# Optimization experiments

Hardware: AMD Instinct MI355X
Metric: run time of the kernel (lower is better)

## Reference

```python
import jax, jax.numpy as jnp
import numpy as np

# Model dims (match init_kwargs)
B, S = 2, 2048          # batch, seq_len
H = 1024                # hidden_size
D = 2048                # expert_hidden_dim
E = 8                   # num_experts
K = 2                   # num_experts_per_tok (top_k)


def setup_inputs() -> dict:
    key = jax.random.key(0)
    k_x, k_g, k_w1, k_w2 = jax.random.split(key, 4)
    x = jax.random.normal(k_x, (B, S, H), jnp.float32)
    # router gate: Linear(H, E, bias=False)
    gate_w = jax.random.normal(k_g, (H, E), jnp.float32) / jnp.sqrt(H).astype(jnp.float32)
    # per-expert FFN params stacked on leading expert axis
    W1 = jax.random.normal(k_w1, (E, H, D), jnp.float32) / jnp.sqrt(H).astype(jnp.float32)
    b1 = jnp.zeros((E, D), jnp.float32)
    W2 = jax.random.normal(k_w2, (E, D, H), jnp.float32) / jnp.sqrt(D).astype(jnp.float32)
    b2 = jnp.zeros((E, H), jnp.float32)
    return {"x": x, "gate_w": gate_w, "W1": W1, "b1": b1, "W2": W2, "b2": b2}


def reference(x, gate_w, W1, b1, W2, b2):
    # --- router ---
    logits = jnp.einsum('bsh,he->bse', x, gate_w)            # [B,S,E]
    probs = jax.nn.softmax(logits, axis=-1)                  # [B,S,E]
    topk_p, idx = jax.lax.top_k(probs, K)                    # [B,S,K] each
    topk_p = topk_p / topk_p.sum(axis=-1, keepdims=True)     # renormalize over top-k
    one_hot = jax.nn.one_hot(idx, E, dtype=probs.dtype)      # [B,S,K,E]
    # combine weight per (token, expert); topk indices are distinct so this
    # equals the original's masked-sum of router_probs_flat * expert_mask
    combine = jnp.einsum('bske,bsk->bse', one_hot, topk_p)   # [B,S,E]

    # --- aux load-balancing loss (faithful to original reductions) ---
    tokens_per_expert = one_hot.sum(axis=-2).mean(axis=0)    # [S,E]
    avg_prob_per_expert = probs.mean(axis=(0, 1))            # [E]
    aux_loss = E * (tokens_per_expert * avg_prob_per_expert).sum()

    # --- experts: dense-equivalent of gather-FFN-scatter (tokens with
    # combine weight 0 contribute 0, matching the masked loop) ---
    out = jnp.zeros_like(x)
    for e in range(E):  # fixed small loop over structurally distinct experts
        h = jax.nn.gelu(jnp.einsum('bsh,hd->bsd', x, W1[e]) + b1[e], approximate=False)
        out = out + combine[..., e:e + 1] * (jnp.einsum('bsd,dh->bsh', h, W2[e]) + b2[e])
    return out, aux_loss
```

## Files before the change

kernel.cpp:

```cpp
#include <hip/hip_runtime.h>
#include <hip/hip_bf16.h>

#define NTOK 4096
#define HD   1024
#define DD   2048
#define NE   8
#define SLOTS (2*NTOK)

typedef unsigned short u16;
typedef unsigned int   u32;
typedef __attribute__((ext_vector_type(8))) __bf16 bf16x8;
typedef __attribute__((ext_vector_type(4))) float  f32x4;

__device__ __forceinline__ float bf2f(u16 u) {
    u32 v = ((u32)u) << 16;
    return __uint_as_float(v);
}
__device__ __forceinline__ u16 f2bf(float f) {
    __hip_bfloat16 h = __float2bfloat16(f);
    return *reinterpret_cast<u16*>(&h);
}

__device__ __forceinline__ void gload_lds16(const void* g, void* l) {
    __builtin_amdgcn_global_load_lds(
        (__attribute__((address_space(1))) void*)g,
        (__attribute__((address_space(3))) void*)l,
        16, 0, 0);
}

__device__ __forceinline__ float gelu_f(float v) {
    float x = 0.7978845608028654f * (v + 0.044715f * v * v * v);
    float e = exp2f(x * 2.8853900817779268f);
    float th = 1.f - 2.f * __builtin_amdgcn_rcpf(e + 1.f);
    return 0.5f * v * (1.f + th);
}

__global__ __launch_bounds__(256) void cvt2_k(
        const float* __restrict__ W1, const float* __restrict__ W2,
        u16* __restrict__ W1t, u16* __restrict__ W2t) {
    int z = blockIdx.z;
    const float* src; u16* dst; int R, C;
    if (z < NE) { src = W1 + (size_t)z * HD * DD;        dst = W1t + (size_t)z * HD * DD;        R = HD; C = DD; }
    else        { src = W2 + (size_t)(z - NE) * DD * HD; dst = W2t + (size_t)(z - NE) * DD * HD; R = DD; C = HD; }
    int tcols = C >> 6;
    int r0 = (blockIdx.x / tcols) * 64;
    int c0 = (blockIdx.x % tcols) * 64;

    __shared__ u16 tile[64][68];
    int tid = threadIdx.x;
    int rr  = tid >> 4;
    int cc4 = (tid & 15) * 4;
#pragma unroll
    for (int j = 0; j < 4; ++j) {
        int r = rr + j * 16;
        float4 v = *reinterpret_cast<const float4*>(src + (size_t)(r0 + r) * C + c0 + cc4);
        tile[r][cc4 + 0] = f2bf(v.x); tile[r][cc4 + 1] = f2bf(v.y);
        tile[r][cc4 + 2] = f2bf(v.z); tile[r][cc4 + 3] = f2bf(v.w);
    }
    __syncthreads();
    int cc = tid >> 3, sl = tid & 7;
#pragma unroll
    for (int p = 0; p < 2; ++p) {
        int c = p * 32 + cc;
        u16 tmp[8];
#pragma unroll
        for (int k = 0; k < 8; ++k) tmp[k] = tile[sl * 8 + k][c];
        *reinterpret_cast<uint4*>(dst + (size_t)(c0 + c) * R + r0 + sl * 8) =
            *reinterpret_cast<uint4*>(tmp);
    }
}

__global__ __launch_bounds__(256) void router_k(
        const float* __restrict__ x, const float* __restrict__ gw,
        u16* __restrict__ xb,
        int* __restrict__ counts, float* __restrict__ sum_probs,
        int* __restrict__ tk_idx, float* __restrict__ tk_w) {
    __shared__ int   bcnt[NE];
    __shared__ float bprob[NE];
    int tid = threadIdx.x;
    if (tid < NE) { bcnt[tid] = 0; bprob[tid] = 0.f; }
    __syncthreads();

    int gtid = blockIdx.x * 256 + tid;
    int t    = gtid >> 6;
    int lane = gtid & 63;

    float acc[NE] = {0.f,0.f,0.f,0.f,0.f,0.f,0.f,0.f};
    const float* xr = x + (size_t)t * HD;
    u16* xbr = xb + (size_t)t * HD;
#pragma unroll
    for (int i = 0; i < HD / 64; ++i) {
        int h = lane + i * 64;
        float xv = xr[h];
        xbr[h] = f2bf(xv);
        const float4* g = reinterpret_cast<const float4*>(gw + (size_t)h * NE);
        float4 g0 = g[0], g1 = g[1];
        acc[0] = fmaf(xv, g0.x, acc[0]); acc[1] = fmaf(xv, g0.y, acc[1]);
        acc[2] = fmaf(xv, g0.z, acc[2]); acc[3] = fmaf(xv, g0.w, acc[3]);
        acc[4] = fmaf(xv, g1.x, acc[4]); acc[5] = fmaf(xv, g1.y, acc[5]);
        acc[6] = fmaf(xv, g1.z, acc[6]); acc[7] = fmaf(xv, g1.w, acc[7]);
    }
#pragma unroll
    for (int off = 32; off >= 1; off >>= 1) {
#pragma unroll
        for (int e = 0; e < NE; ++e) acc[e] += __shfl_xor(acc[e], off);
    }
    float m = acc[0];
#pragma unroll
    for (int e = 1; e < NE; ++e) m = fmaxf(m, acc[e]);
    float p[NE]; float s = 0.f;
#pragma unroll
    for (int e = 0; e < NE; ++e) { p[e] = expf(acc[e] - m); s += p[e]; }
    float inv = 1.f / s;

    int i1 = 0; float v1 = p[0];
#pragma unroll
    for (int e = 1; e < NE; ++e) if (p[e] > v1) { v1 = p[e]; i1 = e; }
    int i2 = -1; float v2 = -1.f;
#pragma unroll
    for (int e = 0; e < NE; ++e) if (e != i1 && p[e] > v2) { v2 = p[e]; i2 = e; }
    float wsum = v1 + v2;

    if (lane < NE) atomicAdd(&bprob[lane], p[lane] * inv);
    if (lane == 0) {
        atomicAdd(&bcnt[i1], 1);
        atomicAdd(&bcnt[i2], 1);
        tk_idx[2 * t]     = i1;  tk_idx[2 * t + 1] = i2;
        tk_w[2 * t]       = v1 / wsum;
        tk_w[2 * t + 1]   = v2 / wsum;
    }
    __syncthreads();
    if (tid < NE) {
        if (bcnt[tid]) atomicAdd(&counts[tid], bcnt[tid]);
        atomicAdd(&sum_probs[tid], bprob[tid]);
    }
}

__global__ __launch_bounds__(256) void scatter_k(
        const int* __restrict__ tk_idx, const int* __restrict__ counts,
        int* __restrict__ cursor, int* __restrict__ slot_tok,
        int* __restrict__ inv_slot, int* __restrict__ offsets) {
    __shared__ int off[NE];
    if (threadIdx.x == 0) {
        int o = 0;
        for (int e = 0; e < NE; ++e) { off[e] = o; o += counts[e]; }
        if (blockIdx.x == 0)
            for (int e = 0; e < NE; ++e) offsets[e] = off[e];
    }
    __syncthreads();
    int t = blockIdx.x * 256 + threadIdx.x;
    if (t >= NTOK) return;
#pragma unroll
    for (int k = 0; k < 2; ++k) {
        int e = tk_idx[2 * t + k];
        int pos = atomicAdd(&cursor[e], 1);
        int s = off[e] + pos;
        slot_tok[s] = t;
        inv_slot[2 * t + k] = s;
    }
}

template<int KD, bool GATHER, bool GELU>
__global__ __launch_bounds__(256) void gemm_dense_k(
        const u16* __restrict__ A,
        const u16* __restrict__ Bt,
        const float* __restrict__ bias,
        const int* __restrict__ counts, const int* __restrict__ offsets,
        const int* __restrict__ slot_tok,
        u16* __restrict__ outb, int ND) {
    int mb = blockIdx.y;
    int e = -1, m0 = 0, accb = 0;
#pragma unroll
    for (int ee = 0; ee < NE; ++ee) {
        int nb = (counts[ee] + 127) >> 7;
        if (e < 0 && mb < accb + nb) { e = ee; m0 = (mb - accb) * 128; }
        accb += nb;
    }
    if (e < 0) return;
    int cnt = counts[e], base = offsets[e];
    int n0 = blockIdx.x * 128;

    __shared__ u16 As[128 * 64];
    __shared__ u16 Bs[128 * 64];
    __shared__ int ids[128];

    int tid  = threadIdx.x;
    int lane = tid & 63;
    int w    = tid >> 6;
    int wr   = w >> 1, wc = w & 1;
    int lrow = lane & 15, khi = lane >> 4;

    if constexpr (GATHER) {
        if (tid < 128) ids[tid] = (m0 + tid < cnt) ? slot_tok[base + m0 + tid] : 0;
    }
    __syncthreads();

    const u16* Bte = Bt + (size_t)e * (size_t)ND * KD;
    int srow = tid >> 3;
    int sslot = tid & 7;

    const u16 *gA[4], *gB[4];
#pragma unroll
    for (int j = 0; j < 4; ++j) {
        int r = j * 32 + srow;
        size_t gr;
        if constexpr (GATHER) gr = (size_t)ids[r];
        else                  gr = (size_t)(base + m0 + r);
        gA[j] = A   + gr * KD                + ((sslot ^ (r & 7)) << 3);
        gB[j] = Bte + (size_t)(n0 + r) * KD  + ((sslot ^ (r & 7)) << 3);
    }

    f32x4 acc[4][4];
#pragma unroll
    for (int m = 0; m < 4; ++m)
#pragma unroll
        for (int n = 0; n < 4; ++n) acc[m][n] = {0.f, 0.f, 0.f, 0.f};

    constexpr int NK = KD / 64;
#pragma unroll 1
    for (int t = 0; t < NK; ++t) {
#pragma unroll
        for (int j = 0; j < 4; ++j) {
            gload_lds16(gA[j] + t * 64, (char*)As + j * 4096 + tid * 16);
            gload_lds16(gB[j] + t * 64, (char*)Bs + j * 4096 + tid * 16);
        }
        __syncthreads();
#pragma unroll
        for (int ks = 0; ks < 2; ++ks) {
            int slot = ks * 4 + khi;
            bf16x8 af[4], bv[4];
#pragma unroll
            for (int m = 0; m < 4; ++m) {
                int r = wr * 64 + m * 16 + lrow;
                af[m] = *reinterpret_cast<const bf16x8*>(
                    &As[r * 64 + ((slot ^ (r & 7)) << 3)]);
            }
#pragma unroll
            for (int n = 0; n < 4; ++n) {
                int r = wc * 64 + n * 16 + lrow;
                bv[n] = *reinterpret_cast<const bf16x8*>(
                    &Bs[r * 64 + ((slot ^ (r & 7)) << 3)]);
            }
            __builtin_amdgcn_s_setprio(1);
#pragma unroll
            for (int m = 0; m < 4; ++m)
#pragma unroll
                for (int n = 0; n < 4; ++n)
                    acc[m][n] = __builtin_amdgcn_mfma_f32_16x16x32_bf16(
                        af[m], bv[n], acc[m][n], 0, 0, 0);
            __builtin_amdgcn_s_setprio(0);
        }
        __syncthreads();
    }

    constexpr int PST = 72;
    u16* patch = As + w * 16 * PST;
    float bvals[4];
    if constexpr (GELU) {
#pragma unroll
        for (int n = 0; n < 4; ++n)
            bvals[n] = bias[(size_t)e * ND + n0 + wc * 64 + n * 16 + lrow];
    }
#pragma unroll
    for (int m = 0; m < 4; ++m) {
#pragma unroll
        for (int n = 0; n < 4; ++n)
#pragma unroll
            for (int i = 0; i < 4; ++i) {
                float v = acc[m][n][i];
                if constexpr (GELU) {
                    v += bvals[n];
                    v = gelu_f(v);
                }
                patch[(khi * 4 + i) * PST + n * 16 + lrow] = f2bf(v);
            }
        __syncthreads();
        int prow = lane >> 3, sl = lane & 7;
#pragma unroll
        for (int p = 0; p < 2; ++p) {
            int row  = p * 8 + prow;
            uint4 q = *reinterpret_cast<const uint4*>(&patch[row * PST + sl * 8]);
            int grow = m0 + wr * 64 + m * 16 + row;
            if (grow < cnt)
                *reinterpret_cast<uint4*>(
                    outb + (size_t)(base + grow) * ND + n0 + wc * 64 + sl * 8) = q;
        }
        __syncthreads();
    }
}

template<int KD>
__global__ __launch_bounds__(256) void gemm_n64_k(
        const u16* __restrict__ A,
        const u16* __restrict__ Bt,
        const int* __restrict__ counts, const int* __restrict__ offsets,
        u16* __restrict__ outb, int ND) {
    int mb = blockIdx.y;
    int e = -1, m0 = 0, accb = 0;
#pragma unroll
    for (int ee = 0; ee < NE; ++ee) {
        int nb = (counts[ee] + 127) >> 7;
        if (e < 0 && mb < accb + nb) { e = ee; m0 = (mb - accb) * 128; }
        accb += nb;
    }
    if (e < 0) return;
    int cnt = counts[e], base = offsets[e];
    int n0 = blockIdx.x * 64;

    __shared__ u16 As[128 * 64];
    __shared__ u16 Bs[64 * 64];

    int tid  = threadIdx.x;
    int lane = tid & 63;
    int w    = tid >> 6;
    int wr   = w >> 1, wc = w & 1;
    int lrow = lane & 15, khi = lane >> 4;

    const u16* Bte = Bt + (size_t)e * (size_t)ND * KD;
    int srow = tid >> 3;
    int sslot = tid & 7;

    const u16 *gA[4], *gB[2];
#pragma unroll
    for (int j = 0; j < 4; ++j) {
        int r = j * 32 + srow;
        gA[j] = A + (size_t)(base + m0 + r) * KD + ((sslot ^ (r & 7)) << 3);
    }
#pragma unroll
    for (int j = 0; j < 2; ++j) {
        int r = j * 32 + srow;
        gB[j] = Bte + (size_t)(n0 + r) * KD + ((sslot ^ (r & 7)) << 3);
    }

    f32x4 acc[4][2];
#pragma unroll
    for (int m = 0; m < 4; ++m)
#pragma unroll
        for (int n = 0; n < 2; ++n) acc[m][n] = {0.f, 0.f, 0.f, 0.f};

    constexpr int NK = KD / 64;
#pragma unroll 1
    for (int t = 0; t < NK; ++t) {
#pragma unroll
        for (int j = 0; j < 4; ++j)
            gload_lds16(gA[j] + t * 64, (char*)As + j * 4096 + tid * 16);
#pragma unroll
        for (int j = 0; j < 2; ++j)
            gload_lds16(gB[j] + t * 64, (char*)Bs + j * 4096 + tid * 16);
        __syncthreads();
#pragma unroll
        for (int ks = 0; ks < 2; ++ks) {
            int slot = ks * 4 + khi;
            bf16x8 af[4], bv[2];
#pragma unroll
            for (int m = 0; m < 4; ++m) {
                int r = wr * 64 + m * 16 + lrow;
                af[m] = *reinterpret_cast<const bf16x8*>(
                    &As[r * 64 + ((slot ^ (r & 7)) << 3)]);
            }
#pragma unroll
            for (int n = 0; n < 2; ++n) {
                int r = wc * 32 + n * 16 + lrow;
                bv[n] = *reinterpret_cast<const bf16x8*>(
                    &Bs[r * 64 + ((slot ^ (r & 7)) << 3)]);
            }
            __builtin_amdgcn_s_setprio(1);
#pragma unroll
            for (int m = 0; m < 4; ++m)
#pragma unroll
                for (int n = 0; n < 2; ++n)
                    acc[m][n] = __builtin_amdgcn_mfma_f32_16x16x32_bf16(
                        af[m], bv[n], acc[m][n], 0, 0, 0);
            __builtin_amdgcn_s_setprio(0);
        }
        __syncthreads();
    }

    constexpr int PST = 40;
    u16* patch = As + w * 16 * PST;
#pragma unroll
    for (int m = 0; m < 4; ++m) {
#pragma unroll
        for (int n = 0; n < 2; ++n)
#pragma unroll
            for (int i = 0; i < 4; ++i)
                patch[(khi * 4 + i) * PST + n * 16 + lrow] = f2bf(acc[m][n][i]);
        __syncthreads();
        int row = lane >> 2, sl = lane & 3;
        uint4 q = *reinterpret_cast<const uint4*>(&patch[row * PST + sl * 8]);
        int grow = m0 + wr * 64 + m * 16 + row;
        if (grow < cnt)
            *reinterpret_cast<uint4*>(
                outb + (size_t)(base + grow) * ND + n0 + wc * 32 + sl * 8) = q;
        __syncthreads();
    }
}

__global__ __launch_bounds__(256) void combine_k(
        const int* __restrict__ tk_idx, const float* __restrict__ tk_w,
        const int* __restrict__ inv_slot, const u16* __restrict__ ybuf,
        const float* __restrict__ b2, float* __restrict__ out,
        const int* __restrict__ counts, const float* __restrict__ sum_probs,
        float* __restrict__ out_aux) {
    if (blockIdx.x == 0 && threadIdx.x == 0) {
        double s = 0.0;
        for (int e = 0; e < NE; ++e) s += (double)counts[e] * (double)sum_probs[e];
        out_aux[0] = (float)(s * (8.0 / (2.0 * (double)NTOK)));
    }
    int gtid = blockIdx.x * 256 + threadIdx.x;
    int t = gtid >> 6;
    int lane = gtid & 63;
    int e0 = tk_idx[2 * t], e1 = tk_idx[2 * t + 1];
    float w0 = tk_w[2 * t], w1 = tk_w[2 * t + 1];
    int s0 = inv_slot[2 * t], s1 = inv_slot[2 * t + 1];

#pragma unroll
    for (int i = 0; i < 2; ++i) {
        int c = lane * 8 + i * 512;
        uint4 q0 = *reinterpret_cast<const uint4*>(ybuf + (size_t)s0 * HD + c);
        uint4 q1 = *reinterpret_cast<const uint4*>(ybuf + (size_t)s1 * HD + c);
        float y0[8] = {bf2f((u16)(q0.x&0xffff)), bf2f((u16)(q0.x>>16)),
                       bf2f((u16)(q0.y&0xffff)), bf2f((u16)(q0.y>>16)),
                       bf2f((u16)(q0.z&0xffff)), bf2f((u16)(q0.z>>16)),
                       bf2f((u16)(q0.w&0xffff)), bf2f((u16)(q0.w>>16))};
        float y1[8] = {bf2f((u16)(q1.x&0xffff)), bf2f((u16)(q1.x>>16)),
                       bf2f((u16)(q1.y&0xffff)), bf2f((u16)(q1.y>>16)),
                       bf2f((u16)(q1.z&0xffff)), bf2f((u16)(q1.z>>16)),
                       bf2f((u16)(q1.w&0xffff)), bf2f((u16)(q1.w>>16))};
        float r[8];
#pragma unroll
        for (int j = 0; j < 8; ++j) {
            float v0 = y0[j] + b2[e0 * HD + c + j];
            float v1 = y1[j] + b2[e1 * HD + c + j];
            r[j] = w0 * v0 + w1 * v1;
        }
        float* op = out + (size_t)t * HD + c;
        *reinterpret_cast<float4*>(op)     = make_float4(r[0], r[1], r[2], r[3]);
        *reinterpret_cast<float4*>(op + 4) = make_float4(r[4], r[5], r[6], r[7]);
    }
}

extern "C" void kernel_launch(void* const* d_in, const int* in_sizes, int n_in,
                              void* d_out, int out_size, void* d_ws, size_t ws_size,
                              hipStream_t stream) {
    const float* x   = (const float*)d_in[0];
    const float* gw  = (const float*)d_in[1];
    const float* W1  = (const float*)d_in[2];
    const float* b1  = (const float*)d_in[3];
    const float* W2  = (const float*)d_in[4];
    const float* b2  = (const float*)d_in[5];
    float* out = (float*)d_out;

    char* ws = (char*)d_ws;
    int*   counts    = (int*)(ws + 0);
    int*   cursor    = (int*)(ws + 32);
    int*   offsets   = (int*)(ws + 64);
    float* sum_probs = (float*)(ws + 128);
    int*   tk_idx    = (int*)(ws + 512);
    float* tk_w      = (float*)(ws + 33280);
    int*   slot_tok  = (int*)(ws + 66048);
    int*   inv_slot  = (int*)(ws + 98816);
    u16*   xb        = (u16*)(ws + 131584);
    u16*   W1t       = (u16*)(ws + 8520192);
    u16*   W2t       = (u16*)(ws + 42074624);
    u16*   hbuf      = (u16*)(ws + 75629056);
    u16*   ybuf      = W1t;

    hipMemsetAsync(ws, 0, 512, stream);

    cvt2_k<<<dim3(512, 1, 2 * NE), 256, 0, stream>>>(W1, W2, W1t, W2t);
    router_k<<<NTOK / 4, 256, 0, stream>>>(x, gw, xb, counts, sum_probs, tk_idx, tk_w);
    scatter_k<<<NTOK / 256, 256, 0, stream>>>(tk_idx, counts, cursor,
                                              slot_tok, inv_slot, offsets);

    gemm_dense_k<HD, true, true><<<dim3(DD / 128, 72, 1), 256, 0, stream>>>(
        xb, W1t, b1, counts, offsets, slot_tok, hbuf, DD);
    gemm_n64_k<DD><<<dim3(HD / 64, 72, 1), 256, 0, stream>>>(
        hbuf, W2t, counts, offsets, ybuf, HD);

    combine_k<<<NTOK / 4, 256, 0, stream>>>(tk_idx, tk_w, inv_slot, ybuf, b2, out,
                                            counts, sum_probs,
                                            out + (size_t)NTOK * HD);
}
```

Baseline: 215.4 us.

## Fuse weight conversion with router, widen GEMM1 tiles, add XCD-aware block mapping

Merges the weight convert/transpose kernel and the router into one launch, which removes a kernel boundary. The first expert GEMM now uses 512-thread blocks with 128x256 tiles, so each A tile is reused across twice as many output columns. Both GEMMs now map a 1D grid so that the blocks on each XCD (blockIdx & 7) share the same M rows, aiming for better L2 locality. The trade-off is more LDS and fewer blocks for GEMM1, which may lower occupancy.

```diff
diff --git a/kernel.cpp b/kernel.cpp
--- a/kernel.cpp
+++ b/kernel.cpp
@@ -35,53 +35,54 @@
     return 0.5f * v * (1.f + th);
 }
 
-__global__ __launch_bounds__(256) void cvt2_k(
+__global__ __launch_bounds__(256) void prep_k(
         const float* __restrict__ W1, const float* __restrict__ W2,
-        u16* __restrict__ W1t, u16* __restrict__ W2t) {
-    int z = blockIdx.z;
-    const float* src; u16* dst; int R, C;
-    if (z < NE) { src = W1 + (size_t)z * HD * DD;        dst = W1t + (size_t)z * HD * DD;        R = HD; C = DD; }
-    else        { src = W2 + (size_t)(z - NE) * DD * HD; dst = W2t + (size_t)(z - NE) * DD * HD; R = DD; C = HD; }
-    int tcols = C >> 6;
-    int r0 = (blockIdx.x / tcols) * 64;
-    int c0 = (blockIdx.x % tcols) * 64;
-
-    __shared__ u16 tile[64][68];
-    int tid = threadIdx.x;
-    int rr  = tid >> 4;
-    int cc4 = (tid & 15) * 4;
-#pragma unroll
-    for (int j = 0; j < 4; ++j) {
-        int r = rr + j * 16;
-        float4 v = *reinterpret_cast<const float4*>(src + (size_t)(r0 + r) * C + c0 + cc4);
-        tile[r][cc4 + 0] = f2bf(v.x); tile[r][cc4 + 1] = f2bf(v.y);
-        tile[r][cc4 + 2] = f2bf(v.z); tile[r][cc4 + 3] = f2bf(v.w);
-    }
-    __syncthreads();
-    int cc = tid >> 3, sl = tid & 7;
-#pragma unroll
-    for (int p = 0; p < 2; ++p) {
-        int c = p * 32 + cc;
-        u16 tmp[8];
-#pragma unroll
-        for (int k = 0; k < 8; ++k) tmp[k] = tile[sl * 8 + k][c];
-        *reinterpret_cast<uint4*>(dst + (size_t)(c0 + c) * R + r0 + sl * 8) =
-            *reinterpret_cast<uint4*>(tmp);
-    }
-}
-
-__global__ __launch_bounds__(256) void router_k(
+        u16* __restrict__ W1t, u16* __restrict__ W2t,
         const float* __restrict__ x, const float* __restrict__ gw,
         u16* __restrict__ xb,
         int* __restrict__ counts, float* __restrict__ sum_probs,
         int* __restrict__ tk_idx, float* __restrict__ tk_w) {
+    int bid = blockIdx.x;
+    int tid = threadIdx.x;
+    if (bid < 8192) {
+        int z  = bid >> 9;
+        int xq = bid & 511;
+        const float* src; u16* dst; int R, C;
+        if (z < NE) { src = W1 + (size_t)z * HD * DD;        dst = W1t + (size_t)z * HD * DD;        R = HD; C = DD; }
+        else        { src = W2 + (size_t)(z - NE) * DD * HD; dst = W2t + (size_t)(z - NE) * DD * HD; R = DD; C = HD; }
+        int tcols = C >> 6;
+        int r0 = (xq / tcols) * 64;
+        int c0 = (xq % tcols) * 64;
+
+        __shared__ u16 tile[64][68];
+        int rr  = tid >> 4;
+        int cc4 = (tid & 15) * 4;
+#pragma unroll
+        for (int j = 0; j < 4; ++j) {
+            int r = rr + j * 16;
+            float4 v = *reinterpret_cast<const float4*>(src + (size_t)(r0 + r) * C + c0 + cc4);
+            tile[r][cc4 + 0] = f2bf(v.x); tile[r][cc4 + 1] = f2bf(v.y);
+            tile[r][cc4 + 2] = f2bf(v.z); tile[r][cc4 + 3] = f2bf(v.w);
+        }
+        __syncthreads();
+        int cc = tid >> 3, sl = tid & 7;
+#pragma unroll
+        for (int p = 0; p < 2; ++p) {
+            int c = p * 32 + cc;
+            u16 tmp[8];
+#pragma unroll
+            for (int k = 0; k < 8; ++k) tmp[k] = tile[sl * 8 + k][c];
+            *reinterpret_cast<uint4*>(dst + (size_t)(c0 + c) * R + r0 + sl * 8) =
+                *reinterpret_cast<uint4*>(tmp);
+        }
+        return;
+    }
     __shared__ int   bcnt[NE];
     __shared__ float bprob[NE];
-    int tid = threadIdx.x;
     if (tid < NE) { bcnt[tid] = 0; bprob[tid] = 0.f; }
     __syncthreads();
 
-    int gtid = blockIdx.x * 256 + tid;
+    int gtid = (bid - 8192) * 256 + tid;
     int t    = gtid >> 6;
     int lane = gtid & 63;
 
@@ -161,14 +162,17 @@
 }
 
 template<int KD, bool GATHER, bool GELU>
-__global__ __launch_bounds__(256) void gemm_dense_k(
+__global__ __launch_bounds__(512) void gemm_wide_k(
         const u16* __restrict__ A,
         const u16* __restrict__ Bt,
         const float* __restrict__ bias,
         const int* __restrict__ counts, const int* __restrict__ offsets,
         const int* __restrict__ slot_tok,
         u16* __restrict__ outb, int ND) {
-    int mb = blockIdx.y;
+    int xcd = blockIdx.x & 7;
+    int s   = blockIdx.x >> 3;
+    int mb  = xcd * 9 + (s >> 3);
+    int nx  = s & 7;
     int e = -1, m0 = 0, accb = 0;
 #pragma unroll
     for (int ee = 0; ee < NE; ++ee) {
@@ -178,16 +182,17 @@
     }
     if (e < 0) return;
     int cnt = counts[e], base = offsets[e];
-    int n0 = blockIdx.x * 128;
-
-    __shared__ u16 As[128 * 64];
-    __shared__ u16 Bs[128 * 64];
+    int n0 = nx * 256;
+
+    __shared__ u16 smem[(128 + 256) * 64];
     __shared__ int ids[128];
+    u16* As = smem;
+    u16* Bs = smem + 128 * 64;
 
     int tid  = threadIdx.x;
     int lane = tid & 63;
     int w    = tid >> 6;
-    int wr   = w >> 1, wc = w & 1;
+    int wr   = w >> 2, wc = w & 3;
     int lrow = lane & 15, khi = lane >> 4;
 
     if constexpr (GATHER) {
@@ -199,15 +204,19 @@
     int srow = tid >> 3;
     int sslot = tid & 7;
 
-    const u16 *gA[4], *gB[4];
-#pragma unroll
-    for (int j = 0; j < 4; ++j) {
-        int r = j * 32 + srow;
+    const u16 *gA[2], *gB[4];
+#pragma unroll
+    for (int j = 0; j < 2; ++j) {
+        int r = j * 64 + srow;
         size_t gr;
         if constexpr (GATHER) gr = (size_t)ids[r];
         else                  gr = (size_t)(base + m0 + r);
-        gA[j] = A   + gr * KD                + ((sslot ^ (r & 7)) << 3);
-        gB[j] = Bte + (size_t)(n0 + r) * KD  + ((sslot ^ (r & 7)) << 3);
+        gA[j] = A + gr * KD + ((sslot ^ (r & 7)) << 3);
+    }
+#pragma unroll
+    for (int j = 0; j < 4; ++j) {
+        int r = j * 64 + srow;
+        gB[j] = Bte + (size_t)(n0 + r) * KD + ((sslot ^ (r & 7)) << 3);
     }
 
     f32x4 acc[4][4];
@@ -220,10 +229,11 @@
 #pragma unroll 1
     for (int t = 0; t < NK; ++t) {
 #pragma unroll
-        for (int j = 0; j < 4; ++j) {
-            gload_lds16(gA[j] + t * 64, (char*)As + j * 4096 + tid * 16);
-            gload_lds16(gB[j] + t * 64, (char*)Bs + j * 4096 + tid * 16);
-        }
+        for (int j = 0; j < 2; ++j)
+            gload_lds16(gA[j] + t * 64, (char*)As + j * 8192 + tid * 16);
+#pragma unroll
+        for (int j = 0; j < 4; ++j)
+            gload_lds16(gB[j] + t * 64, (char*)Bs + j * 8192 + tid * 16);
         __syncthreads();
 #pragma unroll
         for (int ks = 0; ks < 2; ++ks) {
@@ -254,7 +264,7 @@
     }
 
     constexpr int PST = 72;
-    u16* patch = As + w * 16 * PST;
+    u16* patch = smem + w * 16 * PST;
     float bvals[4];
     if constexpr (GELU) {
 #pragma unroll
@@ -295,7 +305,10 @@
         const u16* __restrict__ Bt,
         const int* __restrict__ counts, const int* __restrict__ offsets,
         u16* __restrict__ outb, int ND) {
-    int mb = blockIdx.y;
+    int xcd = blockIdx.x & 7;
+    int s   = blockIdx.x >> 3;
+    int mb  = xcd * 9 + (s >> 4);
+    int nx  = s & 15;
     int e = -1, m0 = 0, accb = 0;
 #pragma unroll
     for (int ee = 0; ee < NE; ++ee) {
@@ -305,7 +318,7 @@
     }
     if (e < 0) return;
     int cnt = counts[e], base = offsets[e];
-    int n0 = blockIdx.x * 64;
+    int n0 = nx * 64;
 
     __shared__ u16 As[128 * 64];
     __shared__ u16 Bs[64 * 64];
@@ -468,14 +481,15 @@
 
     hipMemsetAsync(ws, 0, 512, stream);
 
-    cvt2_k<<<dim3(512, 1, 2 * NE), 256, 0, stream>>>(W1, W2, W1t, W2t);
-    router_k<<<NTOK / 4, 256, 0, stream>>>(x, gw, xb, counts, sum_probs, tk_idx, tk_w);
+    prep_k<<<8192 + 1024, 256, 0, stream>>>(W1, W2, W1t, W2t,
+                                            x, gw, xb, counts, sum_probs,
+                                            tk_idx, tk_w);
     scatter_k<<<NTOK / 256, 256, 0, stream>>>(tk_idx, counts, cursor,
                                               slot_tok, inv_slot, offsets);
 
-    gemm_dense_k<HD, true, true><<<dim3(DD / 128, 72, 1), 256, 0, stream>>>(
+    gemm_wide_k<HD, true, true><<<576, 512, 0, stream>>>(
         xb, W1t, b1, counts, offsets, slot_tok, hbuf, DD);
-    gemm_n64_k<DD><<<dim3(HD / 64, 72, 1), 256, 0, stream>>>(
+    gemm_n64_k<DD><<<1152, 256, 0, stream>>>(
         hbuf, W2t, counts, offsets, ybuf, HD);
 
     combine_k<<<NTOK / 4, 256, 0, stream>>>(tk_idx, tk_w, inv_slot, ybuf, b2, out,
```

Result: faster. 211.2 us (-2.0%).
